# Performance work log

Measured on AMD Instinct MI355X. Metric: run time of the kernel, lower is better.

The kernel has to match this reference:

```python
import jax, jax.numpy as jnp
import numpy as np

# Loss hyperparameters (match init_kwargs)
DELTA_VAR = 0.75
DELTA_DIST = 2.0
ALPHA, BETA, GAMMA = 1.0, 1.0, 0.001


def setup_inputs() -> dict:
    key = jax.random.key(0)
    k1, k2 = jax.random.split(key)
    B, C, H, W = 4, 32, 512, 512
    N_INST = 100
    input_ = jax.random.normal(k1, (B, C, H, W), dtype=jnp.float32)
    target = jax.random.randint(k2, (B, 1, H, W), 0, N_INST, dtype=jnp.int64)
    return {"input_": input_, "target": target, "n_instances": N_INST}


def _loss_single(feat, lbl, n_inst):
    # feat: [C, H, W] embeddings for one sample; lbl: [H, W] instance ids in [0, n_inst)
    C = feat.shape[0]
    f = feat.reshape(C, -1).T                     # [P, C] pixel embeddings
    l = lbl.reshape(-1)                           # [P]
    counts = jnp.bincount(l, length=n_inst).astype(f.dtype)     # [n]
    sums = jax.ops.segment_sum(f, l, num_segments=n_inst)       # [n, C]
    means = sums / counts[:, None]                               # cluster means [n, C]

    # variance (attractive) term: hinge on distance of each pixel to its cluster mean
    diff = f - means[l]                           # gather means back to pixels
    var = jnp.linalg.norm(diff, axis=1)           # 'fro' over dim=1 == L2
    var = jnp.clip(var - DELTA_VAR, 0.0) ** 2 / counts[l]
    variance_term = var.sum() / n_inst

    # distance (repulsive) term: hinged pairwise distances between cluster means
    eye = jnp.eye(n_inst, dtype=f.dtype)
    d2 = jnp.sum((means[:, None, :] - means[None, :, :]) ** 2, axis=2)  # [n, n]
    # safe sqrt: diagonal is exactly 0; mask it so grads stay finite, value unchanged
    dmat = jnp.sqrt(jnp.where(d2 > 0, d2, 1.0)) * (1.0 - eye)
    repulsion = 2.0 * DELTA_DIST * (1.0 - eye)
    hinged = jnp.clip(repulsion - dmat, 0.0) ** 2
    distance_term = hinged.sum() / (n_inst * (n_inst - 1))

    # regularization term: pull cluster means toward origin
    reg_term = jnp.linalg.norm(means, axis=1).sum() / n_inst

    return ALPHA * variance_term + BETA * distance_term + GAMMA * reg_term


def reference(input_, target, n_instances):
    # input_: [B, C, H, W], target: [B, 1, H, W]
    lbl = target[:, 0]
    losses = jax.vmap(lambda f, l: _loss_single(f, l, n_instances))(input_, lbl)
    return losses.mean()  # loss.div(n_batches)
```

## Files before the change

kernel.cpp:

```cpp
#include <hip/hip_runtime.h>
#include <math.h>

#define BB 4
#define CC 32
#define HWSZ (512*512)
#define NMAX 128
#define NP 132
#define PPB 2048
#define CHUNKS (HWSZ / PPB)
#define DELTA_VAR_C 0.75f
#define DELTA_DIST_C 2.0f
#define GAMMA_C 0.001f
#define FXS 1048576.0f
#define FXI (1.0f / 1048576.0f)

#define LD4(p) (*(const float4*)(p))

__device__ __forceinline__ float block_reduce_256(float v, float* red, int tid) {
    #pragma unroll
    for (int o = 32; o > 0; o >>= 1) v += __shfl_down(v, o, 64);
    if ((tid & 63) == 0) red[tid >> 6] = v;
    __syncthreads();
    if (tid == 0) v = red[0] + red[1] + red[2] + red[3];
    return v;
}

__global__ __launch_bounds__(256) void k_seg_sum(
    const float* __restrict__ in, const int* __restrict__ lbl,
    const int* __restrict__ n_ptr, int* __restrict__ sums_i,
    unsigned int* __restrict__ counts_u)
{
    const int N = *n_ptr;
    __shared__ int s_sum[CC * NP];
    __shared__ unsigned int s_cnt[NMAX];
    const int tid = threadIdx.x;

    for (int i = tid; i < CC * NP; i += 256) s_sum[i] = 0;
    for (int i = tid; i < NMAX; i += 256) s_cnt[i] = 0u;
    __syncthreads();

    const int b = blockIdx.x >> 7;
    const int p0 = (blockIdx.x & (CHUNKS - 1)) * PPB;

    const float* inb = in + (size_t)b * CC * HWSZ;
    const int* lb = lbl + (size_t)b * HWSZ + p0 + tid * 8;

    int4 l4a = *(const int4*)(lb);
    int4 l4b = *(const int4*)(lb + 4);
    int lab[8] = {l4a.x, l4a.y, l4a.z, l4a.w, l4b.x, l4b.y, l4b.z, l4b.w};

    #pragma unroll
    for (int i = 0; i < 8; i++) atomicAdd(&s_cnt[lab[i]], 1u);

    const float* p = inb + p0 + (size_t)tid * 8;
    float4 a0 = LD4(p);            float4 b0 = LD4(p + 4);
    float4 a1 = LD4(p + HWSZ);     float4 b1 = LD4(p + HWSZ + 4);

    for (int c = 0; c < CC; c += 2) {
        float4 ca0 = a0, cb0 = b0, ca1 = a1, cb1 = b1;
        if (c + 2 < CC) {
            const float* q = p + (size_t)(c + 2) * HWSZ;
            a0 = LD4(q);          b0 = LD4(q + 4);
            a1 = LD4(q + HWSZ);   b1 = LD4(q + HWSZ + 4);
        }
        float v0[8] = {ca0.x, ca0.y, ca0.z, ca0.w, cb0.x, cb0.y, cb0.z, cb0.w};
        #pragma unroll
        for (int i = 0; i < 8; i++)
            atomicAdd(&s_sum[c * NP + lab[i]], (int)rintf(v0[i] * FXS));
        float v1[8] = {ca1.x, ca1.y, ca1.z, ca1.w, cb1.x, cb1.y, cb1.z, cb1.w};
        #pragma unroll
        for (int i = 0; i < 8; i++)
            atomicAdd(&s_sum[(c + 1) * NP + lab[i]], (int)rintf(v1[i] * FXS));
    }
    __syncthreads();

    for (int i = tid; i < N * CC; i += 256) {
        int n = i / CC, c = i % CC;
        int val = s_sum[c * NP + n];
        if (val != 0) atomicAdd(&sums_i[(size_t)b * NMAX * CC + i], val);
    }
    for (int i = tid; i < N; i += 256) {
        unsigned int cv = s_cnt[i];
        if (cv) atomicAdd(&counts_u[b * NMAX + i], cv);
    }
}

__global__ __launch_bounds__(256) void k_means(
    const int* __restrict__ sums_i, const unsigned int* __restrict__ counts_u,
    const int* __restrict__ n_ptr, float* __restrict__ means)
{
    const int N = *n_ptr;
    const int b = blockIdx.x;
    const int tid = threadIdx.x;
    for (int i = tid; i < N * CC; i += 256) {
        int n = i / CC;
        float mu = (float)sums_i[(size_t)b * NMAX * CC + i] * FXI
                 / (float)counts_u[b * NMAX + n];
        means[(size_t)b * NMAX * CC + i] = mu;
    }
}

#define DSLICE 8
__global__ __launch_bounds__(256) void k_dist(
    const float* __restrict__ means, const int* __restrict__ n_ptr,
    int* __restrict__ out_acc)
{
    const int N = *n_ptr;
    const int b = blockIdx.x / DSLICE;
    const int slice = blockIdx.x % DSLICE;
    __shared__ float m[NMAX * 33];
    __shared__ float red[4];
    const int tid = threadIdx.x;

    for (int i = tid; i < N * CC; i += 256)
        m[(i / CC) * 33 + (i % CC)] = means[(size_t)b * NMAX * CC + i];
    __syncthreads();

    float dist_sum = 0.f;
    for (int pr = slice * 256 + tid; pr < N * N; pr += DSLICE * 256) {
        int i = pr / N, j = pr - i * N;
        if (i == j) continue;
        float d2 = 0.f;
        #pragma unroll
        for (int c = 0; c < CC; c++) {
            float d = m[i * 33 + c] - m[j * 33 + c];
            d2 += d * d;
        }
        float dm = (d2 > 0.f) ? sqrtf(d2) : 1.0f;
        float h = fmaxf(2.0f * DELTA_DIST_C - dm, 0.f);
        dist_sum += h * h;
    }
    float acc = dist_sum / ((float)N * (float)(N - 1));
    if (slice == 0) {
        float reg_sum = 0.f;
        for (int n = tid; n < N; n += 256) {
            float s = 0.f;
            #pragma unroll
            for (int c = 0; c < CC; c++) { float v = m[n * 33 + c]; s += v * v; }
            reg_sum += sqrtf(s);
        }
        acc += reg_sum * (GAMMA_C / (float)N);
    }
    float tot = block_reduce_256(acc, red, tid);
    if (tid == 0)
        atomicAdd(out_acc, (int)rintf(tot * (1.0f / (float)BB) * FXS));
}

__global__ __launch_bounds__(256) void k_var(
    const float* __restrict__ in, const int* __restrict__ lbl,
    const int* __restrict__ n_ptr, const float* __restrict__ means,
    const unsigned int* __restrict__ counts_u, int* __restrict__ out_acc)
{
    const int N = *n_ptr;
    __shared__ float m_t[CC * NP];
    __shared__ float invc[NMAX];
    __shared__ float red[4];
    const int tid = threadIdx.x;

    const int b = blockIdx.x >> 7;
    const int p0 = (blockIdx.x & (CHUNKS - 1)) * PPB;

    for (int i = tid; i < N * CC; i += 256) {
        int n = i / CC, c = i % CC;
        m_t[c * NP + n] = means[(size_t)b * NMAX * CC + i];
    }
    for (int i = tid; i < N; i += 256)
        invc[i] = 1.0f / (float)counts_u[b * NMAX + i];
    __syncthreads();

    const float* inb = in + (size_t)b * CC * HWSZ;
    const int* lb = lbl + (size_t)b * HWSZ + p0 + tid * 8;

    int4 l4a = *(const int4*)(lb);
    int4 l4b = *(const int4*)(lb + 4);
    int lab[8] = {l4a.x, l4a.y, l4a.z, l4a.w, l4b.x, l4b.y, l4b.z, l4b.w};
    float acc[8] = {0.f, 0.f, 0.f, 0.f, 0.f, 0.f, 0.f, 0.f};

    const float* p = inb + p0 + (size_t)tid * 8;
    float4 a0 = LD4(p);            float4 b0 = LD4(p + 4);
    float4 a1 = LD4(p + HWSZ);     float4 b1 = LD4(p + HWSZ + 4);

    for (int c = 0; c < CC; c += 2) {
        float4 ca0 = a0, cb0 = b0, ca1 = a1, cb1 = b1;
        if (c + 2 < CC) {
            const float* q = p + (size_t)(c + 2) * HWSZ;
            a0 = LD4(q);          b0 = LD4(q + 4);
            a1 = LD4(q + HWSZ);   b1 = LD4(q + HWSZ + 4);
        }
        float v0[8] = {ca0.x, ca0.y, ca0.z, ca0.w, cb0.x, cb0.y, cb0.z, cb0.w};
        #pragma unroll
        for (int i = 0; i < 8; i++) {
            float d = v0[i] - m_t[c * NP + lab[i]];
            acc[i] += d * d;
        }
        float v1[8] = {ca1.x, ca1.y, ca1.z, ca1.w, cb1.x, cb1.y, cb1.z, cb1.w};
        #pragma unroll
        for (int i = 0; i < 8; i++) {
            float d = v1[i] - m_t[(c + 1) * NP + lab[i]];
            acc[i] += d * d;
        }
    }

    float vsum = 0.f;
    #pragma unroll
    for (int i = 0; i < 8; i++) {
        float nm = sqrtf(acc[i]);
        float t = fmaxf(nm - DELTA_VAR_C, 0.f);
        vsum += t * t * invc[lab[i]];
    }
    float tot = block_reduce_256(vsum, red, tid);
    if (tid == 0)
        atomicAdd(out_acc, (int)rintf(tot * (1.0f / ((float)N * (float)BB)) * FXS));
}

__global__ void k_final(const int* __restrict__ out_acc, float* __restrict__ out) {
    if (threadIdx.x == 0 && blockIdx.x == 0)
        *out = (float)(*out_acc) * FXI;
}

extern "C" void kernel_launch(void* const* d_in, const int* in_sizes, int n_in,
                              void* d_out, int out_size, void* d_ws, size_t ws_size,
                              hipStream_t stream) {
    (void)in_sizes; (void)n_in; (void)out_size; (void)ws_size;
    const float* in  = (const float*)d_in[0];
    const int*   lbl = (const int*)d_in[1];
    const int*   n_ptr = (const int*)d_in[2];
    float* out = (float*)d_out;

    int* sums_i = (int*)d_ws;
    unsigned int* counts_u = (unsigned int*)(sums_i + BB * NMAX * CC);
    int* out_acc = (int*)(counts_u + BB * NMAX);
    float* means = (float*)(out_acc + 1);

    hipMemsetAsync(d_ws, 0,
                   (size_t)(BB * NMAX * CC + BB * NMAX + 1) * sizeof(int), stream);

    const int blocks = BB * CHUNKS;
    k_seg_sum<<<blocks, 256, 0, stream>>>(in, lbl, n_ptr, sums_i, counts_u);
    k_means<<<BB, 256, 0, stream>>>(sums_i, counts_u, n_ptr, means);
    k_var<<<blocks, 256, 0, stream>>>(in, lbl, n_ptr, means, counts_u, out_acc);
    k_dist<<<BB * DSLICE, 256, 0, stream>>>(means, n_ptr, out_acc);
    k_final<<<1, 64, 0, stream>>>(out_acc, out);
}
```

Baseline: 235.7 us.

## Pack channel pairs into 64-bit LDS atomics and fuse means/distance into variance kernel

```diff
diff --git a/kernel.cpp b/kernel.cpp
--- a/kernel.cpp
+++ b/kernel.cpp
@@ -6,13 +6,21 @@
 #define HWSZ (512*512)
 #define NMAX 128
 #define NP 132
+#define NP64 133
+#define SS (NMAX * CC)
+
 #define PPB 2048
 #define CHUNKS (HWSZ / PPB)
+#define NBLK (BB * CHUNKS)
+
+#define DSLICE 8
+
 #define DELTA_VAR_C 0.75f
 #define DELTA_DIST_C 2.0f
 #define GAMMA_C 0.001f
 #define FXS 1048576.0f
 #define FXI (1.0f / 1048576.0f)
+#define BIAS 16777216
 
 #define LD4(p) (*(const float4*)(p))
 
@@ -31,20 +39,18 @@
     unsigned int* __restrict__ counts_u)
 {
     const int N = *n_ptr;
-    __shared__ int s_sum[CC * NP];
+    __shared__ unsigned long long s_sum[(CC / 2) * NP64];
     __shared__ unsigned int s_cnt[NMAX];
     const int tid = threadIdx.x;
 
-    for (int i = tid; i < CC * NP; i += 256) s_sum[i] = 0;
+    for (int i = tid; i < (CC / 2) * NP64; i += 256) s_sum[i] = 0ull;
     for (int i = tid; i < NMAX; i += 256) s_cnt[i] = 0u;
     __syncthreads();
 
-    const int b = blockIdx.x >> 7;
-    const int p0 = (blockIdx.x & (CHUNKS - 1)) * PPB;
-
-    const float* inb = in + (size_t)b * CC * HWSZ;
+    const int b = blockIdx.x / CHUNKS;
+    const int p0 = (blockIdx.x % CHUNKS) * PPB;
+
     const int* lb = lbl + (size_t)b * HWSZ + p0 + tid * 8;
-
     int4 l4a = *(const int4*)(lb);
     int4 l4b = *(const int4*)(lb + 4);
     int lab[8] = {l4a.x, l4a.y, l4a.z, l4a.w, l4b.x, l4b.y, l4b.z, l4b.w};
@@ -52,7 +58,8 @@
     #pragma unroll
     for (int i = 0; i < 8; i++) atomicAdd(&s_cnt[lab[i]], 1u);
 
-    const float* p = inb + p0 + (size_t)tid * 8;
+    const float* p = in + (size_t)b * CC * HWSZ + p0 + (size_t)tid * 8;
+
     float4 a0 = LD4(p);            float4 b0 = LD4(p + 4);
     float4 a1 = LD4(p + HWSZ);     float4 b1 = LD4(p + HWSZ + 4);
 
@@ -64,20 +71,26 @@
             a1 = LD4(q + HWSZ);   b1 = LD4(q + HWSZ + 4);
         }
         float v0[8] = {ca0.x, ca0.y, ca0.z, ca0.w, cb0.x, cb0.y, cb0.z, cb0.w};
+        float v1[8] = {ca1.x, ca1.y, ca1.z, ca1.w, cb1.x, cb1.y, cb1.z, cb1.w};
+        unsigned long long* row = &s_sum[(c >> 1) * NP64];
         #pragma unroll
-        for (int i = 0; i < 8; i++)
-            atomicAdd(&s_sum[c * NP + lab[i]], (int)rintf(v0[i] * FXS));
-        float v1[8] = {ca1.x, ca1.y, ca1.z, ca1.w, cb1.x, cb1.y, cb1.z, cb1.w};
-        #pragma unroll
-        for (int i = 0; i < 8; i++)
-            atomicAdd(&s_sum[(c + 1) * NP + lab[i]], (int)rintf(v1[i] * FXS));
+        for (int i = 0; i < 8; i++) {
+            unsigned int lo = (unsigned int)((int)(v0[i] * FXS) + BIAS);
+            unsigned int hi = (unsigned int)((int)(v1[i] * FXS) + BIAS);
+            unsigned long long pk = (unsigned long long)lo |
+                                    ((unsigned long long)hi << 32);
+            atomicAdd(&row[lab[i]], pk);
+        }
     }
     __syncthreads();
 
     for (int i = tid; i < N * CC; i += 256) {
         int n = i / CC, c = i % CC;
-        int val = s_sum[c * NP + n];
-        if (val != 0) atomicAdd(&sums_i[(size_t)b * NMAX * CC + i], val);
+        unsigned long long v = s_sum[(c >> 1) * NP64 + n];
+        unsigned int half = (c & 1) ? (unsigned int)(v >> 32) : (unsigned int)v;
+        long long val = (long long)half - ((long long)s_cnt[n] << 24);
+        if (val != 0)
+            atomicAdd(&sums_i[(size_t)b * SS + i], (int)val);
     }
     for (int i = tid; i < N; i += 256) {
         unsigned int cv = s_cnt[i];
@@ -85,98 +98,37 @@
     }
 }
 
-__global__ __launch_bounds__(256) void k_means(
-    const int* __restrict__ sums_i, const unsigned int* __restrict__ counts_u,
-    const int* __restrict__ n_ptr, float* __restrict__ means)
-{
-    const int N = *n_ptr;
-    const int b = blockIdx.x;
-    const int tid = threadIdx.x;
-    for (int i = tid; i < N * CC; i += 256) {
-        int n = i / CC;
-        float mu = (float)sums_i[(size_t)b * NMAX * CC + i] * FXI
-                 / (float)counts_u[b * NMAX + n];
-        means[(size_t)b * NMAX * CC + i] = mu;
-    }
-}
-
-#define DSLICE 8
-__global__ __launch_bounds__(256) void k_dist(
-    const float* __restrict__ means, const int* __restrict__ n_ptr,
-    int* __restrict__ out_acc)
-{
-    const int N = *n_ptr;
-    const int b = blockIdx.x / DSLICE;
-    const int slice = blockIdx.x % DSLICE;
-    __shared__ float m[NMAX * 33];
-    __shared__ float red[4];
-    const int tid = threadIdx.x;
-
-    for (int i = tid; i < N * CC; i += 256)
-        m[(i / CC) * 33 + (i % CC)] = means[(size_t)b * NMAX * CC + i];
-    __syncthreads();
-
-    float dist_sum = 0.f;
-    for (int pr = slice * 256 + tid; pr < N * N; pr += DSLICE * 256) {
-        int i = pr / N, j = pr - i * N;
-        if (i == j) continue;
-        float d2 = 0.f;
-        #pragma unroll
-        for (int c = 0; c < CC; c++) {
-            float d = m[i * 33 + c] - m[j * 33 + c];
-            d2 += d * d;
-        }
-        float dm = (d2 > 0.f) ? sqrtf(d2) : 1.0f;
-        float h = fmaxf(2.0f * DELTA_DIST_C - dm, 0.f);
-        dist_sum += h * h;
-    }
-    float acc = dist_sum / ((float)N * (float)(N - 1));
-    if (slice == 0) {
-        float reg_sum = 0.f;
-        for (int n = tid; n < N; n += 256) {
-            float s = 0.f;
-            #pragma unroll
-            for (int c = 0; c < CC; c++) { float v = m[n * 33 + c]; s += v * v; }
-            reg_sum += sqrtf(s);
-        }
-        acc += reg_sum * (GAMMA_C / (float)N);
-    }
-    float tot = block_reduce_256(acc, red, tid);
-    if (tid == 0)
-        atomicAdd(out_acc, (int)rintf(tot * (1.0f / (float)BB) * FXS));
-}
-
 __global__ __launch_bounds__(256) void k_var(
     const float* __restrict__ in, const int* __restrict__ lbl,
-    const int* __restrict__ n_ptr, const float* __restrict__ means,
+    const int* __restrict__ n_ptr, const int* __restrict__ sums_i,
     const unsigned int* __restrict__ counts_u, int* __restrict__ out_acc)
 {
     const int N = *n_ptr;
     __shared__ float m_t[CC * NP];
-    __shared__ float invc[NMAX];
+    __shared__ float s_invc[NMAX];
     __shared__ float red[4];
     const int tid = threadIdx.x;
 
-    const int b = blockIdx.x >> 7;
-    const int p0 = (blockIdx.x & (CHUNKS - 1)) * PPB;
-
+    const int b = blockIdx.x / CHUNKS;
+    const int chunk = blockIdx.x % CHUNKS;
+    const int p0 = chunk * PPB;
+
+    for (int i = tid; i < N; i += 256)
+        s_invc[i] = 1.0f / (float)counts_u[b * NMAX + i];
+    __syncthreads();
     for (int i = tid; i < N * CC; i += 256) {
         int n = i / CC, c = i % CC;
-        m_t[c * NP + n] = means[(size_t)b * NMAX * CC + i];
-    }
-    for (int i = tid; i < N; i += 256)
-        invc[i] = 1.0f / (float)counts_u[b * NMAX + i];
-    __syncthreads();
-
-    const float* inb = in + (size_t)b * CC * HWSZ;
+        m_t[c * NP + n] = (float)sums_i[(size_t)b * SS + i] * FXI * s_invc[n];
+    }
+    __syncthreads();
+
     const int* lb = lbl + (size_t)b * HWSZ + p0 + tid * 8;
-
     int4 l4a = *(const int4*)(lb);
     int4 l4b = *(const int4*)(lb + 4);
     int lab[8] = {l4a.x, l4a.y, l4a.z, l4a.w, l4b.x, l4b.y, l4b.z, l4b.w};
     float acc[8] = {0.f, 0.f, 0.f, 0.f, 0.f, 0.f, 0.f, 0.f};
 
-    const float* p = inb + p0 + (size_t)tid * 8;
+    const float* p = in + (size_t)b * CC * HWSZ + p0 + (size_t)tid * 8;
     float4 a0 = LD4(p);            float4 b0 = LD4(p + 4);
     float4 a1 = LD4(p + HWSZ);     float4 b1 = LD4(p + HWSZ + 4);
 
@@ -206,11 +158,41 @@
     for (int i = 0; i < 8; i++) {
         float nm = sqrtf(acc[i]);
         float t = fmaxf(nm - DELTA_VAR_C, 0.f);
-        vsum += t * t * invc[lab[i]];
-    }
-    float tot = block_reduce_256(vsum, red, tid);
+        vsum += t * t * s_invc[lab[i]];
+    }
+    float total = vsum * (1.0f / ((float)N * (float)BB));
+
+    if (chunk < DSLICE) {
+        float dist_sum = 0.f;
+        for (int pr = chunk * 256 + tid; pr < N * N; pr += DSLICE * 256) {
+            int i = pr / N, j = pr - i * N;
+            if (i == j) continue;
+            float d2 = 0.f;
+            #pragma unroll
+            for (int c = 0; c < CC; c++) {
+                float d = m_t[c * NP + i] - m_t[c * NP + j];
+                d2 += d * d;
+            }
+            float dm = (d2 > 0.f) ? sqrtf(d2) : 1.0f;
+            float h = fmaxf(2.0f * DELTA_DIST_C - dm, 0.f);
+            dist_sum += h * h;
+        }
+        total += dist_sum * (1.0f / ((float)N * (float)(N - 1) * (float)BB));
+        if (chunk == 0) {
+            float reg_sum = 0.f;
+            for (int n = tid; n < N; n += 256) {
+                float s = 0.f;
+                #pragma unroll
+                for (int c = 0; c < CC; c++) { float v = m_t[c * NP + n]; s += v * v; }
+                reg_sum += sqrtf(s);
+            }
+            total += reg_sum * (GAMMA_C / ((float)N * (float)BB));
+        }
+    }
+
+    float tot = block_reduce_256(total, red, tid);
     if (tid == 0)
-        atomicAdd(out_acc, (int)rintf(tot * (1.0f / ((float)N * (float)BB)) * FXS));
+        atomicAdd(out_acc, (int)rintf(tot * FXS));
 }
 
 __global__ void k_final(const int* __restrict__ out_acc, float* __restrict__ out) {
@@ -228,17 +210,12 @@
     float* out = (float*)d_out;
 
     int* sums_i = (int*)d_ws;
-    unsigned int* counts_u = (unsigned int*)(sums_i + BB * NMAX * CC);
+    unsigned int* counts_u = (unsigned int*)(sums_i + BB * SS);
     int* out_acc = (int*)(counts_u + BB * NMAX);
-    float* means = (float*)(out_acc + 1);
-
-    hipMemsetAsync(d_ws, 0,
-                   (size_t)(BB * NMAX * CC + BB * NMAX + 1) * sizeof(int), stream);
-
-    const int blocks = BB * CHUNKS;
-    k_seg_sum<<<blocks, 256, 0, stream>>>(in, lbl, n_ptr, sums_i, counts_u);
-    k_means<<<BB, 256, 0, stream>>>(sums_i, counts_u, n_ptr, means);
-    k_var<<<blocks, 256, 0, stream>>>(in, lbl, n_ptr, means, counts_u, out_acc);
-    k_dist<<<BB * DSLICE, 256, 0, stream>>>(means, n_ptr, out_acc);
+
+    hipMemsetAsync(d_ws, 0, (size_t)(BB * SS + BB * NMAX + 1) * sizeof(int), stream);
+
+    k_seg_sum<<<NBLK, 256, 0, stream>>>(in, lbl, n_ptr, sums_i, counts_u);
+    k_var<<<NBLK, 256, 0, stream>>>(in, lbl, n_ptr, sums_i, counts_u, out_acc);
     k_final<<<1, 64, 0, stream>>>(out_acc, out);
 }
```

Measured after the change: 225.3 us. 1.05x faster.
